# Performance work log

Hardware: AMD Instinct MI355X
Metric: run time of the kernel (lower is better)

The kernel has to match this reference:

```python
import jax, jax.numpy as jnp
import numpy as np

B = 65536
X_DIM = 32
H_DIM = 128


def setup_inputs() -> dict:
    key = jax.random.key(0)
    ks = jax.random.split(key, 11)
    f_scale = 0.1
    x = jax.random.uniform(ks[0], (B, X_DIM), dtype=jnp.float32)
    z = jax.random.normal(ks[1], (B, X_DIM), dtype=jnp.float32)
    # M: rand*0.2 with zero diagonal (use_mask=True, empty dag_seed)
    M = jax.random.uniform(ks[2], (X_DIM, X_DIM), dtype=jnp.float32) * 0.2
    M = M * (1.0 - jnp.eye(X_DIM, dtype=jnp.float32))
    # per-node input linears fc_i: weight [h, x_dim+1], column i zeroed (1e-16)
    Wi = jax.random.normal(ks[3], (X_DIM, H_DIM, X_DIM + 1), dtype=jnp.float32) * f_scale * 0.1
    col_mask = 1.0 - jnp.eye(X_DIM + 1, dtype=jnp.float32)[:X_DIM]  # [x_dim, x_dim+1]
    Wi = Wi * col_mask[:, None, :] + 1e-16 * (1.0 - col_mask)[:, None, :]
    bi = jax.random.normal(ks[4], (X_DIM, H_DIM), dtype=jnp.float32) * 0.01
    wf = jax.random.normal(ks[5], (X_DIM, H_DIM), dtype=jnp.float32) * f_scale * 0.1
    bf = jax.random.normal(ks[6], (X_DIM,), dtype=jnp.float32) * 0.01
    W1 = jax.random.normal(ks[7], (H_DIM, H_DIM), dtype=jnp.float32) * f_scale * 0.1
    b1 = jax.random.normal(ks[8], (H_DIM,), dtype=jnp.float32) * 0.01
    W2 = jax.random.normal(ks[9], (H_DIM, H_DIM), dtype=jnp.float32) * f_scale * 0.1
    b2 = jax.random.normal(ks[10], (H_DIM,), dtype=jnp.float32) * 0.01
    return {"x": x, "z": z, "M": M, "Wi": Wi, "bi": bi, "wf": wf,
            "bf": bf, "W1": W1, "b1": b1, "W2": W2, "b2": b2}


def reference(x, z, M, Wi, bi, wf, bf, W1, b1, W2, b2):
    x_dim = M.shape[0]
    eye = jnp.eye(x_dim, dtype=x.dtype)

    def step(out, xs):
        m_col, oh, Wi_i, bi_i, wf_i, bf_i, z_i = xs
        # x_masked = out * M[:, i]; x_masked[:, i] = 0
        xm = out * (m_col * (1.0 - oh))                       # [B, x_dim]
        # fc_i: cat([x_masked, z_i]) @ W.T + b, then ReLU
        h = jax.nn.relu(xm @ Wi_i[:, :x_dim].T
                        + z_i[:, None] * Wi_i[:, x_dim]
                        + bi_i)                                # [B, h]
        # shared 2-layer MLP
        h = jax.nn.relu(h @ W1.T + b1)
        h = jax.nn.relu(h @ W2.T + b2)
        val = jax.nn.sigmoid(h @ wf_i + bf_i)                  # [B]
        out = out * (1.0 - oh) + val[:, None] * oh             # out[:, i] = val
        return out, None

    xs = (M.T, eye, Wi, bi, wf, bf, z.T)
    out, _ = jax.lax.scan(step, x, xs)
    return out
```

## Files before the change

### kernel.cpp

```cpp
#include <hip/hip_runtime.h>
#include <math.h>

#define XD 32
#define HD 128

typedef float f32x16 __attribute__((ext_vector_type(16)));
typedef int v2i __attribute__((ext_vector_type(2)));
typedef int i32x8 __attribute__((ext_vector_type(8)));

#if __has_builtin(__builtin_amdgcn_cvt_pk_fp8_f32)
#define HAVE_CVT_FP8 1
#endif

static __device__ __forceinline__ unsigned char f2e4m3(float f){
  if (!(f==f)) return 0x7F;
  unsigned u = __float_as_uint(f);
  unsigned s = (u>>24)&0x80;
  float a = fabsf(f);
  if (a >= 464.f) return (unsigned char)(s|0x7E);
  if (a < 0.0009765625f) return (unsigned char)s;
  int e = (int)((u>>23)&0xFF) - 127;
  if (e < -6){
    int m = (int)rintf(ldexpf(a, 9));
    if (m >= 8) return (unsigned char)(s|0x08);
    return (unsigned char)(s|(unsigned)m);
  }
  int m = (int)rintf(ldexpf(a, 3-e));
  if (m == 16){ ++e; m = 8; }
  if (e > 8) return (unsigned char)(s|0x7E);
  return (unsigned char)(s | (unsigned)((e+7)<<3) | (unsigned)(m-8));
}

template<bool HI>
static __device__ __forceinline__ int cvtpk_fp8(float a, float b, int old){
#ifdef HAVE_CVT_FP8
  return __builtin_amdgcn_cvt_pk_fp8_f32(a, b, old, HI);
#else
  int w = (int)f2e4m3(a) | ((int)f2e4m3(b) << 8);
  return HI ? ((old & 0x0000FFFF) | (w << 16)) : ((old & (int)0xFFFF0000) | w);
#endif
}

static __device__ __forceinline__ void plswap(int &x, int &y){
#if __has_builtin(__builtin_amdgcn_permlane32_swap)
  v2i r = __builtin_amdgcn_permlane32_swap(x, y, false, false);
  x = r[0]; y = r[1];
#else
  unsigned lane = threadIdx.x & 63u;
  int sx = __shfl_xor(x, 32, 64);
  int sy = __shfl_xor(y, 32, 64);
  int nx = (lane < 32) ? x : sy;
  int ny = (lane < 32) ? sx : y;
  x = nx; y = ny;
#endif
}

static __device__ __forceinline__ i32x8 c2mx(const f32x16 &ca, const f32x16 &cb){
  i32x8 fr;
#pragma unroll
  for (int q = 0; q < 4; ++q){
    int x = cvtpk_fp8<false>(fmaxf(ca[q*4+0],0.f), fmaxf(ca[q*4+1],0.f), 0);
    x     = cvtpk_fp8<true >(fmaxf(ca[q*4+2],0.f), fmaxf(ca[q*4+3],0.f), x);
    int y = cvtpk_fp8<false>(fmaxf(cb[q*4+0],0.f), fmaxf(cb[q*4+1],0.f), 0);
    y     = cvtpk_fp8<true >(fmaxf(cb[q*4+2],0.f), fmaxf(cb[q*4+3],0.f), y);
    plswap(x, y);
    fr[q*2]   = x;
    fr[q*2+1] = y;
  }
  return fr;
}

static __device__ __forceinline__ f32x16 mfma_mx(i32x8 a, i32x8 b, f32x16 c){
  return __builtin_amdgcn_mfma_scale_f32_32x32x64_f8f6f4(
           a, b, c, 0, 0, 0, 0x7F7F7F7F, 0, 0x7F7F7F7F);
}

static __device__ __forceinline__ void ld8(const float* __restrict__ p, float* dst){
  float4 a = *(const float4*)p, b = *(const float4*)(p+4);
  dst[0]=a.x; dst[1]=a.y; dst[2]=a.z; dst[3]=a.w;
  dst[4]=b.x; dst[5]=b.y; dst[6]=b.z; dst[7]=b.w;
}

static __device__ __forceinline__ f32x16 load_bias16(const float* __restrict__ p, int half){
  f32x16 bv;
#pragma unroll
  for (int rg=0; rg<4; ++rg){
    const float4 t = *(const float4*)(p + rg*8 + half*4);
    bv[rg*4+0]=t.x; bv[rg*4+1]=t.y; bv[rg*4+2]=t.z; bv[rg*4+3]=t.w;
  }
  return bv;
}

__global__ void prep(const float* __restrict__ Wi, const float* __restrict__ bi,
                     const float* __restrict__ W1, const float* __restrict__ b1,
                     const float* __restrict__ W2, const float* __restrict__ b2,
                     const float* __restrict__ M,  const float* __restrict__ wf,
                     unsigned char* __restrict__ wip, unsigned char* __restrict__ w1p,
                     unsigned char* __restrict__ w2p, unsigned char* __restrict__ wfp,
                     float* __restrict__ Mt, float* __restrict__ bi8,
                     float* __restrict__ b1s, float* __restrict__ b2s){
  int b = (int)blockIdx.x;
  int l = (int)threadIdx.x;
  int h = l >> 5, cl = l & 31;
  if (b < 256){
    int i = b >> 3, kt = (b >> 2) & 1, fo = b & 3;
    int row = fo*32 + cl;
    unsigned char bytes[8];
#pragma unroll
    for (int j = 0; j < 8; ++j){
      int k = kt*16 + h*8 + j;
      int src = (k == i) ? XD : k;
      bytes[j] = f2e4m3(8.f * Wi[((size_t)i*HD + row)*(XD+1) + src]);
    }
    long v8; __builtin_memcpy(&v8, bytes, 8);
    *(long*)(wip + ((size_t)b*64 + l)*8) = v8;
  } else if (b < 272){
    const float* W = (b < 264) ? W1 : W2;
    unsigned char* dp = (b < 264) ? w1p : w2p;
    int f = (b - 256) & 7;
    int fo = f >> 1, f2 = f & 1;
    int row = fo*32 + cl;
    union { unsigned char bt[32]; int4 v[2]; } u;
#pragma unroll
    for (int j = 0; j < 32; ++j)
      u.bt[j] = f2e4m3(8.f * W[(size_t)row*HD + f2*64 + h*32 + j]);
    *(int4*)(dp + ((size_t)f*64 + l)*32)      = u.v[0];
    *(int4*)(dp + ((size_t)f*64 + l)*32 + 16) = u.v[1];
  } else if (b < 336){
    int f = b - 272;
    int i = f >> 1, f2 = f & 1;
    union { unsigned char bt[32]; int4 v[2]; } u;
#pragma unroll
    for (int j = 0; j < 32; ++j){
      float v = (cl == 0) ? 64.f * wf[(size_t)i*HD + f2*64 + h*32 + j] : 0.f;
      u.bt[j] = f2e4m3(v);
    }
    *(int4*)(wfp + ((size_t)f*64 + l)*32)      = u.v[0];
    *(int4*)(wfp + ((size_t)f*64 + l)*32 + 16) = u.v[1];
  } else if (b == 336){
#pragma unroll
    for (int t = 0; t < 16; ++t){
      int idx = t*64 + l;
      int i = idx >> 5, k = idx & 31;
      Mt[i*32 + k] = M[k*32 + i];
    }
  } else {
    for (int t = 0; t < 64; ++t){
      int idx = t*64 + l;
      bi8[idx] = 8.f * bi[idx];
    }
#pragma unroll
    for (int t = 0; t < 2; ++t){
      b1s[t*64 + l] = 64.f  * b1[t*64 + l];
      b2s[t*64 + l] = 512.f * b2[t*64 + l];
    }
  }
}

static __device__ __forceinline__ void pack_xb(const float (&st)[16], const float (&mtv)[16],
                                               float zvv, int i, bool hm, long (&xb)[2]){
  int xbi[2][2];
#pragma unroll
  for (int kt = 0; kt < 2; ++kt)
#pragma unroll
    for (int d = 0; d < 2; ++d){
      float v0 = st[kt*8+4*d+0]*mtv[kt*8+4*d+0];
      float v1 = st[kt*8+4*d+1]*mtv[kt*8+4*d+1];
      float v2 = st[kt*8+4*d+2]*mtv[kt*8+4*d+2];
      float v3 = st[kt*8+4*d+3]*mtv[kt*8+4*d+3];
      int w = cvtpk_fp8<false>(v0, v1, 0);
      xbi[kt][d] = cvtpk_fp8<true>(v2, v3, w);
    }
  const int kti = i>>4, di = (i>>2)&1, sh = 8*(i&3);
  const int msk = ~(0xFF << sh);
  int pz = cvtpk_fp8<false>(zvv, 0.f, 0) & 0xFF;
  int ins = pz << sh;
#pragma unroll
  for (int kt = 0; kt < 2; ++kt)
#pragma unroll
    for (int d = 0; d < 2; ++d)
      if (kt == kti && d == di){
        int mod = (xbi[kt][d] & msk) | ins;
        xbi[kt][d] = hm ? mod : xbi[kt][d];
      }
#pragma unroll
  for (int kt = 0; kt < 2; ++kt)
    xb[kt] = (long)(((unsigned long)(unsigned)xbi[kt][0]) |
                    ((unsigned long)(unsigned)xbi[kt][1] << 32));
}

static __device__ __forceinline__ i32x8 ld_mx(const unsigned char* __restrict__ p){
  union { int4 h[2]; i32x8 v; } u;
  u.h[0] = *(const int4*)(p);
  u.h[1] = *(const int4*)(p + 16);
  return u.v;
}

__global__ void __launch_bounds__(64, 1)
genkern(const float* __restrict__ x, const float* __restrict__ z,
        const float* __restrict__ bf,
        const unsigned char* __restrict__ wip, const unsigned char* __restrict__ w1p,
        const unsigned char* __restrict__ w2p, const unsigned char* __restrict__ wfp,
        const float* __restrict__ Mt, const float* __restrict__ bi8,
        const float* __restrict__ b1s, const float* __restrict__ b2s,
        float* __restrict__ out)
{
  const int lane = (int)threadIdx.x;
  const int half = lane >> 5, col = lane & 31;
  const long rbase = (long)blockIdx.x * 64;

  i32x8 w1mx[4][2], w2mx[4][2];
#pragma unroll
  for (int fo = 0; fo < 4; ++fo)
#pragma unroll
    for (int f2 = 0; f2 < 2; ++f2){
      int f = fo*2 + f2;
      w1mx[fo][f2] = ld_mx(w1p + ((size_t)f*64 + lane)*32);
      w2mx[fo][f2] = ld_mx(w2p + ((size_t)f*64 + lane)*32);
    }

  float stA[16], stB[16];
#pragma unroll
  for (int kt = 0; kt < 2; ++kt){
    ld8(x + (rbase + col)*XD + kt*16 + half*8,      &stA[kt*8]);
    ld8(x + (rbase + 32 + col)*XD + kt*16 + half*8, &stB[kt*8]);
  }

  long wif[2][4];
  i32x8 wfx[2];
  float zA, zB;
#pragma unroll
  for (int kt = 0; kt < 2; ++kt)
#pragma unroll
    for (int fo = 0; fo < 4; ++fo)
      wif[kt][fo] = *(const long*)(wip + (((size_t)(kt*4 + fo))*64 + lane)*8);
  wfx[0] = ld_mx(wfp + ((size_t)0*64 + lane)*32);
  wfx[1] = ld_mx(wfp + ((size_t)1*64 + lane)*32);
  zA = z[(rbase + col)*XD + 0];
  zB = z[(rbase + 32 + col)*XD + 0];

#pragma unroll 1
  for (int i = 0; i < XD; ++i){
    const int ip = (i + 1) & (XD - 1);
    const bool hm = (half == ((i>>3)&1));
    const int slot_i = ((i>>4)<<3) | (i&7);
    const float bfv = bf[i];

    float mtv[16];
#pragma unroll
    for (int kt = 0; kt < 2; ++kt)
      ld8(Mt + i*32 + kt*16 + half*8, &mtv[kt*8]);

    long xbA[2], xbB[2];
    pack_xb(stA, mtv, zA, i, hm, xbA);
    pack_xb(stB, mtv, zB, i, hm, xbB);
    zA = z[(rbase + col)*XD + ip];
    zB = z[(rbase + 32 + col)*XD + ip];

    f32x16 accA[4], accB[4];
#pragma unroll
    for (int fo = 0; fo < 4; ++fo){
      f32x16 bc = load_bias16(bi8 + (size_t)i*HD + fo*32, half);
      accA[fo] = __builtin_amdgcn_mfma_f32_32x32x16_fp8_fp8(wif[0][fo], xbA[0], bc, 0,0,0);
      accB[fo] = __builtin_amdgcn_mfma_f32_32x32x16_fp8_fp8(wif[0][fo], xbB[0], bc, 0,0,0);
    }
#pragma unroll
    for (int fo = 0; fo < 4; ++fo){
      accA[fo] = __builtin_amdgcn_mfma_f32_32x32x16_fp8_fp8(wif[1][fo], xbA[1], accA[fo], 0,0,0);
      accB[fo] = __builtin_amdgcn_mfma_f32_32x32x16_fp8_fp8(wif[1][fo], xbB[1], accB[fo], 0,0,0);
    }
#pragma unroll
    for (int kt = 0; kt < 2; ++kt)
#pragma unroll
      for (int fo = 0; fo < 4; ++fo)
        wif[kt][fo] = *(const long*)(wip + (((size_t)(ip*8 + kt*4 + fo))*64 + lane)*8);

    {
      i32x8 mxA0 = c2mx(accA[0], accA[1]);
      i32x8 mxA1 = c2mx(accA[2], accA[3]);
      i32x8 mxB0 = c2mx(accB[0], accB[1]);
      i32x8 mxB1 = c2mx(accB[2], accB[3]);
#pragma unroll
      for (int fo = 0; fo < 4; ++fo){
        f32x16 bc = load_bias16(b1s + fo*32, half);
        accA[fo] = mfma_mx(w1mx[fo][0], mxA0, bc);
        accB[fo] = mfma_mx(w1mx[fo][0], mxB0, bc);
      }
#pragma unroll
      for (int fo = 0; fo < 4; ++fo){
        accA[fo] = mfma_mx(w1mx[fo][1], mxA1, accA[fo]);
        accB[fo] = mfma_mx(w1mx[fo][1], mxB1, accB[fo]);
      }
    }

    {
      i32x8 mxA0 = c2mx(accA[0], accA[1]);
      i32x8 mxA1 = c2mx(accA[2], accA[3]);
      i32x8 mxB0 = c2mx(accB[0], accB[1]);
      i32x8 mxB1 = c2mx(accB[2], accB[3]);
#pragma unroll
      for (int fo = 0; fo < 4; ++fo){
        f32x16 bc = load_bias16(b2s + fo*32, half);
        accA[fo] = mfma_mx(w2mx[fo][0], mxA0, bc);
        accB[fo] = mfma_mx(w2mx[fo][0], mxB0, bc);
      }
#pragma unroll
      for (int fo = 0; fo < 4; ++fo){
        accA[fo] = mfma_mx(w2mx[fo][1], mxA1, accA[fo]);
        accB[fo] = mfma_mx(w2mx[fo][1], mxB1, accB[fo]);
      }
    }

    {
      i32x8 mxA0 = c2mx(accA[0], accA[1]);
      i32x8 mxA1 = c2mx(accA[2], accA[3]);
      i32x8 mxB0 = c2mx(accB[0], accB[1]);
      i32x8 mxB1 = c2mx(accB[2], accB[3]);
      f32x16 eA, eB;
#pragma unroll
      for (int q = 0; q < 16; ++q){ eA[q] = 0.f; eB[q] = 0.f; }
      eA = mfma_mx(wfx[0], mxA0, eA);
      eB = mfma_mx(wfx[0], mxB0, eB);
      eA = mfma_mx(wfx[1], mxA1, eA);
      eB = mfma_mx(wfx[1], mxB1, eB);
      float uA = eA[0], uB = eB[0];
      float sA = __shfl_xor(uA, 32, 64);
      float sB = __shfl_xor(uB, 32, 64);
      float tA = half ? sA : uA;
      float tB = half ? sB : uB;
      float vA = 1.f/(1.f + __expf(-(tA*(1.f/32768.f) + bfv)));
      float vB = 1.f/(1.f + __expf(-(tB*(1.f/32768.f) + bfv)));
#pragma unroll
      for (int s = 0; s < 16; ++s)
        if (s == slot_i){
          stA[s] = hm ? vA : stA[s];
          stB[s] = hm ? vB : stB[s];
        }
    }
    wfx[0] = ld_mx(wfp + ((size_t)(ip*2 + 0)*64 + lane)*32);
    wfx[1] = ld_mx(wfp + ((size_t)(ip*2 + 1)*64 + lane)*32);
  }

#pragma unroll
  for (int kt = 0; kt < 2; ++kt){
    float* pA = out + (rbase + col)*XD + kt*16 + half*8;
    float* pB = out + (rbase + 32 + col)*XD + kt*16 + half*8;
    float4 a, b;
    a.x = stA[kt*8+0]; a.y = stA[kt*8+1]; a.z = stA[kt*8+2]; a.w = stA[kt*8+3];
    b.x = stA[kt*8+4]; b.y = stA[kt*8+5]; b.z = stA[kt*8+6]; b.w = stA[kt*8+7];
    *(float4*)pA = a; *(float4*)(pA+4) = b;
    a.x = stB[kt*8+0]; a.y = stB[kt*8+1]; a.z = stB[kt*8+2]; a.w = stB[kt*8+3];
    b.x = stB[kt*8+4]; b.y = stB[kt*8+5]; b.z = stB[kt*8+6]; b.w = stB[kt*8+7];
    *(float4*)pB = a; *(float4*)(pB+4) = b;
  }
}

extern "C" void kernel_launch(void* const* d_in, const int* in_sizes, int n_in,
                              void* d_out, int out_size, void* d_ws, size_t ws_size,
                              hipStream_t stream){
  (void)in_sizes; (void)n_in; (void)out_size; (void)ws_size;
  const float* x  = (const float*)d_in[0];
  const float* z  = (const float*)d_in[1];
  const float* M  = (const float*)d_in[2];
  const float* Wi = (const float*)d_in[3];
  const float* bi = (const float*)d_in[4];
  const float* wf = (const float*)d_in[5];
  const float* bf = (const float*)d_in[6];
  const float* W1 = (const float*)d_in[7];
  const float* b1 = (const float*)d_in[8];
  const float* W2 = (const float*)d_in[9];
  const float* b2 = (const float*)d_in[10];

  unsigned char* wip = (unsigned char*)d_ws;
  unsigned char* w1p = wip + 131072;
  unsigned char* w2p = w1p + 16384;
  unsigned char* wfp = w2p + 16384;
  float*         Mt  = (float*)(wfp + 131072);
  float*         bi8 = Mt + 1024;
  float*         b1s = bi8 + 4096;
  float*         b2s = b1s + 128;

  prep<<<dim3(338), dim3(64), 0, stream>>>(Wi, bi, W1, b1, W2, b2, M, wf,
                                           wip, w1p, w2p, wfp, Mt, bi8, b1s, b2s);
  genkern<<<dim3(1024), dim3(64), 0, stream>>>(x, z, bf, wip, w1p, w2p, wfp, Mt,
                                               bi8, b1s, b2s, (float*)d_out);
}
```

Baseline: 168.1 us.

## Stage shared MLP weights in LDS and run four waves per block

The W1/W2 FP8 fragments were held in 128 VGPRs per lane. They are now packed in a 16B-interleaved layout, copied once into shared memory by a 256-thread block, and reloaded from LDS for each MFMA. Each block covers 256 rows with four waves, so the grid drops to 256 blocks. This frees registers and shares the weight fetch across waves, at the cost of LDS reads in the inner loop. With only 256 blocks on a 256-CU part, each CU may hold a single block, so occupancy may not actually rise.

```diff
diff --git a/kernel.cpp b/kernel.cpp
--- a/kernel.cpp
+++ b/kernel.cpp
@@ -124,8 +124,8 @@
 #pragma unroll
     for (int j = 0; j < 32; ++j)
       u.bt[j] = f2e4m3(8.f * W[(size_t)row*HD + f2*64 + h*32 + j]);
-    *(int4*)(dp + ((size_t)f*64 + l)*32)      = u.v[0];
-    *(int4*)(dp + ((size_t)f*64 + l)*32 + 16) = u.v[1];
+    *(int4*)(dp + ((size_t)((f*2+0)*64 + l))*16) = u.v[0];
+    *(int4*)(dp + ((size_t)((f*2+1)*64 + l))*16) = u.v[1];
   } else if (b < 336){
     int f = b - 272;
     int i = f >> 1, f2 = f & 1;
@@ -196,7 +196,14 @@
   return u.v;
 }
 
-__global__ void __launch_bounds__(64, 1)
+static __device__ __forceinline__ i32x8 ld_mx_lds(const int4* base, int f, int lane){
+  union { int4 h[2]; i32x8 v; } u;
+  u.h[0] = base[(f*2+0)*64 + lane];
+  u.h[1] = base[(f*2+1)*64 + lane];
+  return u.v;
+}
+
+__global__ void __launch_bounds__(256, 1)
 genkern(const float* __restrict__ x, const float* __restrict__ z,
         const float* __restrict__ bf,
         const unsigned char* __restrict__ wip, const unsigned char* __restrict__ w1p,
@@ -205,19 +212,24 @@
         const float* __restrict__ b1s, const float* __restrict__ b2s,
         float* __restrict__ out)
 {
-  const int lane = (int)threadIdx.x;
+  __shared__ int4 wlds[2048];
+
+  const int tid  = (int)threadIdx.x;
+  const int lane = tid & 63;
+  const int wv   = tid >> 6;
   const int half = lane >> 5, col = lane & 31;
-  const long rbase = (long)blockIdx.x * 64;
-
-  i32x8 w1mx[4][2], w2mx[4][2];
-#pragma unroll
-  for (int fo = 0; fo < 4; ++fo)
-#pragma unroll
-    for (int f2 = 0; f2 < 2; ++f2){
-      int f = fo*2 + f2;
-      w1mx[fo][f2] = ld_mx(w1p + ((size_t)f*64 + lane)*32);
-      w2mx[fo][f2] = ld_mx(w2p + ((size_t)f*64 + lane)*32);
-    }
+  const long rbase = (long)blockIdx.x * 256 + wv * 64;
+
+  {
+    const int4* s1 = (const int4*)w1p;
+    const int4* s2 = (const int4*)w2p;
+#pragma unroll
+    for (int t = 0; t < 4; ++t)
+      wlds[t*256 + tid] = s1[t*256 + tid];
+#pragma unroll
+    for (int t = 0; t < 4; ++t)
+      wlds[1024 + t*256 + tid] = s2[t*256 + tid];
+  }
 
   float stA[16], stB[16];
 #pragma unroll
@@ -225,6 +237,8 @@
     ld8(x + (rbase + col)*XD + kt*16 + half*8,      &stA[kt*8]);
     ld8(x + (rbase + 32 + col)*XD + kt*16 + half*8, &stB[kt*8]);
   }
+
+  __syncthreads();
 
   long wif[2][4];
   i32x8 wfx[2];
@@ -282,14 +296,16 @@
       i32x8 mxB1 = c2mx(accB[2], accB[3]);
 #pragma unroll
       for (int fo = 0; fo < 4; ++fo){
+        i32x8 w = ld_mx_lds(wlds, fo*2+0, lane);
         f32x16 bc = load_bias16(b1s + fo*32, half);
-        accA[fo] = mfma_mx(w1mx[fo][0], mxA0, bc);
-        accB[fo] = mfma_mx(w1mx[fo][0], mxB0, bc);
+        accA[fo] = mfma_mx(w, mxA0, bc);
+        accB[fo] = mfma_mx(w, mxB0, bc);
       }
 #pragma unroll
       for (int fo = 0; fo < 4; ++fo){
-        accA[fo] = mfma_mx(w1mx[fo][1], mxA1, accA[fo]);
-        accB[fo] = mfma_mx(w1mx[fo][1], mxB1, accB[fo]);
+        i32x8 w = ld_mx_lds(wlds, fo*2+1, lane);
+        accA[fo] = mfma_mx(w, mxA1, accA[fo]);
+        accB[fo] = mfma_mx(w, mxB1, accB[fo]);
       }
     }
 
@@ -300,14 +316,16 @@
       i32x8 mxB1 = c2mx(accB[2], accB[3]);
 #pragma unroll
       for (int fo = 0; fo < 4; ++fo){
+        i32x8 w = ld_mx_lds(wlds, 8 + fo*2+0, lane);
         f32x16 bc = load_bias16(b2s + fo*32, half);
-        accA[fo] = mfma_mx(w2mx[fo][0], mxA0, bc);
-        accB[fo] = mfma_mx(w2mx[fo][0], mxB0, bc);
+        accA[fo] = mfma_mx(w, mxA0, bc);
+        accB[fo] = mfma_mx(w, mxB0, bc);
       }
 #pragma unroll
       for (int fo = 0; fo < 4; ++fo){
-        accA[fo] = mfma_mx(w2mx[fo][1], mxA1, accA[fo]);
-        accB[fo] = mfma_mx(w2mx[fo][1], mxB1, accB[fo]);
+        i32x8 w = ld_mx_lds(wlds, 8 + fo*2+1, lane);
+        accA[fo] = mfma_mx(w, mxA1, accA[fo]);
+        accB[fo] = mfma_mx(w, mxB1, accB[fo]);
       }
     }
 
@@ -382,6 +400,6 @@
 
   prep<<<dim3(338), dim3(64), 0, stream>>>(Wi, bi, W1, b1, W2, b2, M, wf,
                                            wip, w1p, w2p, wfp, Mt, bi8, b1s, b2s);
-  genkern<<<dim3(1024), dim3(64), 0, stream>>>(x, z, bf, wip, w1p, w2p, wfp, Mt,
+  genkern<<<dim3(256), dim3(256), 0, stream>>>(x, z, bf, wip, w1p, w2p, wfp, Mt,
                                                bi8, b1s, b2s, (float*)d_out);
 }
```

Result: no change. 169.3 us (+0.7%).
